# Kernel tuning notes

Measured on AMD Instinct MI355X. Metric: run time of the kernel, lower is better.

The kernel has to match this reference:

```python
import jax, jax.numpy as jnp
import numpy as np
from jax import lax

T, B, V, N = 128, 256, 256, 1024


def setup_inputs() -> dict:
    key = jax.random.key(0)
    k1, k2, k3, k4 = jax.random.split(key, 4)
    inputs = jax.random.uniform(k1, (T, B, V), dtype=jnp.float32)
    labels = jax.random.uniform(k2, (T * B, V), dtype=jnp.float32)
    weights = jax.random.normal(k3, (V + N, N), dtype=jnp.float32) * 0.1
    bias = jnp.zeros((N,), dtype=jnp.float32)
    output_weights = jax.random.normal(k4, (N, V), dtype=jnp.float32) * 0.1
    output_bias = jnp.zeros((V,), dtype=jnp.float32)
    return {
        "inputs": inputs,
        "labels": labels,
        "weights": weights,
        "bias": bias,
        "output_weights": output_weights,
        "output_bias": output_bias,
    }


def reference(inputs, labels, weights, bias, output_weights, output_bias):
    t, b, v = inputs.shape
    n = weights.shape[1]
    # split concat-matmul into x@Wx + h@Wh (same math as concat([x,h]) @ W)
    w_x = weights[:v]   # [V, N]
    w_h = weights[v:]   # [N, N]

    def step(h, x):
        h_new = jnp.tanh(x @ w_x + h @ w_h + bias)
        return h_new, h_new

    h0 = jnp.zeros((b, n), dtype=inputs.dtype)
    _, outputs = lax.scan(step, h0, inputs)          # [T, B, N]
    outputs = outputs.reshape(t * b, n)              # concat over time
    logits = outputs @ output_weights + output_bias  # [T*B, V]
    # softmax_cross_entropy_with_logits (soft labels), then mean
    log_p = jax.nn.log_softmax(logits, axis=-1)
    loss = jnp.mean(-jnp.sum(labels * log_p, axis=-1))
    return loss
```

## Files before the change

kernel.cpp:

```cpp
#include <hip/hip_runtime.h>
#include <math.h>

typedef __bf16 bf16;
typedef __attribute__((ext_vector_type(4))) __bf16 bf16x4;
typedef __attribute__((ext_vector_type(8))) __bf16 bf16x8;
typedef __attribute__((ext_vector_type(4))) float f32x4;

#define T_STEPS 128
#define B_SZ    256
#define V_SZ    256
#define N_SZ    1024
#define NROWS   (T_STEPS * B_SZ)
#define LDSS    72
#define RSTR    68
#define NGRP    16
#define NCB     16

__device__ __forceinline__ float fast_tanh(float x) {
    float e = __expf(2.0f * x);
    return 1.0f - 2.0f / (e + 1.0f);
}

__global__ void k_convert(const float* __restrict__ src, bf16* __restrict__ dst, int n) {
    int i = (blockIdx.x * blockDim.x + threadIdx.x) * 4;
    if (i < n) {
        float4 v = *(const float4*)(src + i);
        bf16x4 o;
        o.x = (bf16)v.x; o.y = (bf16)v.y; o.z = (bf16)v.z; o.w = (bf16)v.w;
        *(bf16x4*)(dst + i) = o;
    }
}

__global__ void k_transpose_cvt(const float* __restrict__ src, bf16* __restrict__ dst,
                                int R, int C) {
    __shared__ float tile[32][33];
    int c0 = blockIdx.x * 32;
    int r0 = blockIdx.y * 32;
    int tx = threadIdx.x & 31;
    int ty = threadIdx.x >> 5;
#pragma unroll
    for (int i = 0; i < 32; i += 8)
        tile[ty + i][tx] = src[(size_t)(r0 + ty + i) * C + c0 + tx];
    __syncthreads();
#pragma unroll
    for (int i = 0; i < 32; i += 8)
        dst[(size_t)(c0 + ty + i) * R + r0 + tx] = (bf16)tile[tx][ty + i];
}

__global__ __launch_bounds__(256) void k_xproj(
    const bf16* __restrict__ X, const bf16* __restrict__ Wxt,
    const float* __restrict__ bias, bf16* __restrict__ XH)
{
    __shared__ __align__(16) bf16 As[64 * LDSS];
    __shared__ __align__(16) bf16 Bs[64 * LDSS];
    const int tid  = threadIdx.x;
    const int lane = tid & 63;
    const int w    = tid >> 6;
    const int wm   = (w >> 1) * 32;
    const int wn   = (w & 1) * 32;
    const int quad = lane >> 4;
    const int l15  = lane & 15;
    const int m0 = blockIdx.x * 64;
    const int n0 = blockIdx.y * 64;

    const bf16* Ag = X + (size_t)m0 * V_SZ;
    const bf16* Bg = Wxt + (size_t)n0 * V_SZ;

    f32x4 z = {0.f, 0.f, 0.f, 0.f};
    f32x4 acc00 = z, acc01 = z, acc10 = z, acc11 = z;

    for (int k0 = 0; k0 < V_SZ; k0 += 64) {
        {
            int c = tid, row = c >> 3, col = (c & 7) * 8;
            *(bf16x8*)&As[row * LDSS + col] = *(const bf16x8*)&Ag[(size_t)row * V_SZ + k0 + col];
            *(bf16x8*)&Bs[row * LDSS + col] = *(const bf16x8*)&Bg[(size_t)row * V_SZ + k0 + col];
            c = tid + 256; row = c >> 3; col = (c & 7) * 8;
            *(bf16x8*)&As[row * LDSS + col] = *(const bf16x8*)&Ag[(size_t)row * V_SZ + k0 + col];
            *(bf16x8*)&Bs[row * LDSS + col] = *(const bf16x8*)&Bg[(size_t)row * V_SZ + k0 + col];
        }
        __syncthreads();
#pragma unroll
        for (int kc = 0; kc < 64; kc += 32) {
            bf16x8 a0 = *(const bf16x8*)&As[(wm + l15) * LDSS + kc + quad * 8];
            bf16x8 a1 = *(const bf16x8*)&As[(wm + 16 + l15) * LDSS + kc + quad * 8];
            bf16x8 b0 = *(const bf16x8*)&Bs[(wn + l15) * LDSS + kc + quad * 8];
            bf16x8 b1 = *(const bf16x8*)&Bs[(wn + 16 + l15) * LDSS + kc + quad * 8];
            acc00 = __builtin_amdgcn_mfma_f32_16x16x32_bf16(a0, b0, acc00, 0, 0, 0);
            acc01 = __builtin_amdgcn_mfma_f32_16x16x32_bf16(a0, b1, acc01, 0, 0, 0);
            acc10 = __builtin_amdgcn_mfma_f32_16x16x32_bf16(a1, b0, acc10, 0, 0, 0);
            acc11 = __builtin_amdgcn_mfma_f32_16x16x32_bf16(a1, b1, acc11, 0, 0, 0);
        }
        __syncthreads();
    }
    bf16* Out = XH + (size_t)m0 * N_SZ + n0;
    const f32x4 accs[2][2] = {{acc00, acc01}, {acc10, acc11}};
#pragma unroll
    for (int mi = 0; mi < 2; ++mi)
#pragma unroll
        for (int r = 0; r < 4; ++r) {
            int row = wm + mi * 16 + quad * 4 + r;
            bool is_t0 = (m0 + row) < B_SZ;
#pragma unroll
            for (int ni = 0; ni < 2; ++ni) {
                int col = wn + ni * 16 + l15;
                float pre = accs[mi][ni][r] + bias[n0 + col];
                if (is_t0) pre = fast_tanh(pre);
                Out[(size_t)row * N_SZ + col] = (bf16)pre;
            }
        }
}

__global__ __launch_bounds__(512, 2) void k_rnn(
    const bf16* __restrict__ Wht,
    bf16* __restrict__ XH,
    int* __restrict__ cnt)
{
    __shared__ float red[8 * 16 * RSTR];
    const int tid  = threadIdx.x;
    const int lane = tid & 63;
    const int w    = tid >> 6;
    const int quad = lane >> 4;
    const int l15  = lane & 15;
    const int g  = blockIdx.x >> 4;
    const int c  = blockIdx.x & 15;
    const int m0 = g * 16;
    const int n0 = c * 64;
    const int k0 = w * 128;

    const bf16* Bp = Wht + (size_t)(n0 + l15) * N_SZ + k0 + quad * 8;
    bf16x8 b[4][4];
#pragma unroll
    for (int nt = 0; nt < 4; ++nt)
#pragma unroll
        for (int kc = 0; kc < 4; ++kc)
            b[nt][kc] = *(const bf16x8*)&Bp[(size_t)(nt * 16) * N_SZ + kc * 32];

    const int orow = tid >> 5;
    const int ocol = (tid & 31) * 2;
    uint* XHu = (uint*)XH;

    for (int t = 1; t < T_STEPS; ++t) {
        size_t oidx = (((size_t)t * B_SZ + m0 + orow) * N_SZ + n0 + ocol) >> 1;
        uint xw = __hip_atomic_load(&XHu[oidx], __ATOMIC_RELAXED,
                                    __HIP_MEMORY_SCOPE_AGENT);

        if (t > 1) {
            if (tid == 0) {
                while (__hip_atomic_load(&cnt[g * T_STEPS + t - 1],
                                         __ATOMIC_RELAXED, __HIP_MEMORY_SCOPE_AGENT) < NCB)
                    __builtin_amdgcn_s_sleep(2);
            }
            __syncthreads();
        }

        const bf16* Ap = XH + ((size_t)(t - 1) * B_SZ + m0 + l15) * N_SZ + k0 + quad * 8;
        bf16x8 a[4];
#pragma unroll
        for (int kc = 0; kc < 4; ++kc)
            a[kc] = *(const bf16x8*)&Ap[kc * 32];

        f32x4 z = {0.f, 0.f, 0.f, 0.f};
        f32x4 acc[4] = {z, z, z, z};
#pragma unroll
        for (int kc = 0; kc < 4; ++kc)
#pragma unroll
            for (int nt = 0; nt < 4; ++nt)
                acc[nt] = __builtin_amdgcn_mfma_f32_16x16x32_bf16(a[kc], b[nt][kc],
                                                                  acc[nt], 0, 0, 0);

#pragma unroll
        for (int nt = 0; nt < 4; ++nt)
#pragma unroll
            for (int r = 0; r < 4; ++r)
                red[(w * 16 + quad * 4 + r) * RSTR + nt * 16 + l15] = acc[nt][r];
        __syncthreads();

        float s0 = 0.f, s1 = 0.f;
#pragma unroll
        for (int w2 = 0; w2 < 8; ++w2) {
            float2 v = *(const float2*)&red[(w2 * 16 + orow) * RSTR + ocol];
            s0 += v.x; s1 += v.y;
        }
        bf16 x0 = __builtin_bit_cast(bf16, (unsigned short)(xw & 0xffff));
        bf16 x1 = __builtin_bit_cast(bf16, (unsigned short)(xw >> 16));
        bf16 r0 = (bf16)fast_tanh(s0 + (float)x0);
        bf16 r1 = (bf16)fast_tanh(s1 + (float)x1);
        uint outw = (uint)__builtin_bit_cast(unsigned short, r0)
                  | ((uint)__builtin_bit_cast(unsigned short, r1) << 16);
        __hip_atomic_store(&XHu[oidx], outw, __ATOMIC_RELAXED,
                           __HIP_MEMORY_SCOPE_AGENT);

        asm volatile("s_waitcnt vmcnt(0)" ::: "memory");
        __syncthreads();
        if (tid == 0)
            __hip_atomic_fetch_add(&cnt[g * T_STEPS + t], 1,
                                   __ATOMIC_RELAXED, __HIP_MEMORY_SCOPE_AGENT);
    }
}

__global__ __launch_bounds__(512, 4) void k_loss(
    const bf16* __restrict__ XH,
    const bf16* __restrict__ Wot,
    const float* __restrict__ ob,
    const float* __restrict__ labels,
    float* __restrict__ out)
{
    __shared__ __align__(16) bf16 As[128 * LDSS];
    __shared__ __align__(16) bf16 Bs[256 * LDSS];
    const int tid  = threadIdx.x;
    const int lane = tid & 63;
    const int w    = tid >> 6;
    const int quad = lane >> 4;
    const int l15  = lane & 15;
    const int m0 = blockIdx.x * 128;

    f32x4 z = {0.f, 0.f, 0.f, 0.f};
    f32x4 acc[16];
#pragma unroll
    for (int i = 0; i < 16; ++i) acc[i] = z;

    const bf16* Ag = XH + (size_t)m0 * N_SZ;
    for (int k0 = 0; k0 < N_SZ; k0 += 64) {
#pragma unroll
        for (int c = tid; c < 1024; c += 512) {
            int row = c >> 3, col = (c & 7) * 8;
            *(bf16x8*)&As[row * LDSS + col] = *(const bf16x8*)&Ag[(size_t)row * N_SZ + k0 + col];
        }
#pragma unroll
        for (int c = tid; c < 2048; c += 512) {
            int row = c >> 3, col = (c & 7) * 8;
            *(bf16x8*)&Bs[row * LDSS + col] = *(const bf16x8*)&Wot[(size_t)row * N_SZ + k0 + col];
        }
        __syncthreads();
#pragma unroll
        for (int kc = 0; kc < 64; kc += 32) {
            bf16x8 a = *(const bf16x8*)&As[(w * 16 + l15) * LDSS + kc + quad * 8];
#pragma unroll
            for (int nt = 0; nt < 16; ++nt) {
                bf16x8 b = *(const bf16x8*)&Bs[(nt * 16 + l15) * LDSS + kc + quad * 8];
                acc[nt] = __builtin_amdgcn_mfma_f32_16x16x32_bf16(a, b, acc[nt], 0, 0, 0);
            }
        }
        __syncthreads();
    }

    float obv[16];
#pragma unroll
    for (int nt = 0; nt < 16; ++nt) obv[nt] = ob[nt * 16 + l15];

    float total = 0.f;
#pragma unroll
    for (int r = 0; r < 4; ++r) {
        int row = m0 + w * 16 + quad * 4 + r;
        float vals[16];
        float lmax = -3.0e38f;
#pragma unroll
        for (int nt = 0; nt < 16; ++nt) {
            vals[nt] = acc[nt][r] + obv[nt];
            lmax = fmaxf(lmax, vals[nt]);
        }
#pragma unroll
        for (int s = 1; s < 16; s <<= 1)
            lmax = fmaxf(lmax, __shfl_xor(lmax, s, 64));
        float sume = 0.f, labv = 0.f, labs = 0.f;
        const float* lrow = labels + (size_t)row * V_SZ;
#pragma unroll
        for (int nt = 0; nt < 16; ++nt) {
            sume += __expf(vals[nt] - lmax);
            float lb = lrow[nt * 16 + l15];
            labv += lb * vals[nt];
            labs += lb;
        }
#pragma unroll
        for (int s = 1; s < 16; s <<= 1) {
            sume += __shfl_xor(sume, s, 64);
            labv += __shfl_xor(labv, s, 64);
            labs += __shfl_xor(labs, s, 64);
        }
        float lse = lmax + __logf(sume);
        total += labs * lse - labv;
    }
    if (l15 == 0)
        atomicAdd(out, total * (1.0f / (float)NROWS));
}

extern "C" void kernel_launch(void* const* d_in, const int* in_sizes, int n_in,
                              void* d_out, int out_size, void* d_ws, size_t ws_size,
                              hipStream_t stream)
{
    const float* inputs  = (const float*)d_in[0];
    const float* labels  = (const float*)d_in[1];
    const float* weights = (const float*)d_in[2];
    const float* bias    = (const float*)d_in[3];
    const float* out_w   = (const float*)d_in[4];
    const float* out_b   = (const float*)d_in[5];
    float* out = (float*)d_out;

    char* ws = (char*)d_ws;
    bf16* XH  = (bf16*)ws;  ws += (size_t)NROWS * N_SZ * 2;
    bf16* Xb  = (bf16*)ws;  ws += (size_t)NROWS * V_SZ * 2;
    bf16* Wxt = (bf16*)ws;  ws += (size_t)N_SZ * V_SZ * 2;
    bf16* Wht = (bf16*)ws;  ws += (size_t)N_SZ * N_SZ * 2;
    bf16* Wot = (bf16*)ws;  ws += (size_t)V_SZ * N_SZ * 2;
    int*  cnt = (int*)ws;   ws += (size_t)NGRP * T_STEPS * 4;

    hipMemsetAsync(out, 0, sizeof(float), stream);
    hipMemsetAsync(cnt, 0, (size_t)NGRP * T_STEPS * 4, stream);

    k_convert<<<dim3(NROWS * V_SZ / 1024), 256, 0, stream>>>(inputs, Xb, NROWS * V_SZ);
    k_transpose_cvt<<<dim3(N_SZ / 32, V_SZ / 32), 256, 0, stream>>>(weights, Wxt, V_SZ, N_SZ);
    k_transpose_cvt<<<dim3(N_SZ / 32, N_SZ / 32), 256, 0, stream>>>(
        weights + (size_t)V_SZ * N_SZ, Wht, N_SZ, N_SZ);
    k_transpose_cvt<<<dim3(V_SZ / 32, N_SZ / 32), 256, 0, stream>>>(out_w, Wot, N_SZ, V_SZ);

    k_xproj<<<dim3(NROWS / 64, N_SZ / 64), 256, 0, stream>>>(Xb, Wxt, bias, XH);

    k_rnn<<<dim3(NGRP * NCB), 512, 0, stream>>>(Wht, XH, cnt);

    k_loss<<<dim3(NROWS / 128), 512, 0, stream>>>(XH, Wot, out_b, labels, out);
}
```

Before: 561.1 us.

## Fuse input projection and output logits GEMM into persistent RNN kernel

Removes the separate input-projection GEMM and the output-projection GEMM. Each recurrent block now computes x@Wx on the fly from register-held Wx slices, and uses idle time after publishing h_t to compute the logits slice of h_{t-1}@Wo. The logits go to a bf16 buffer that a lightweight softmax-cross-entropy kernel then reduces. The intent is to cut DRAM traffic and kernel launches by using the latency-bound recurrence's spare compute. The cost is more register pressure and extra LDS reductions and barriers inside every step of the serial loop, plus rounding the logits to bf16.

Result: faster. 502.2 us (-10.5%).

```diff
diff --git a/kernel.cpp b/kernel.cpp
--- a/kernel.cpp
+++ b/kernel.cpp
@@ -11,8 +11,8 @@
 #define V_SZ    256
 #define N_SZ    1024
 #define NROWS   (T_STEPS * B_SZ)
-#define LDSS    72
 #define RSTR    68
+#define LSTR    17
 #define NGRP    16
 #define NCB     16
 
@@ -47,75 +47,18 @@
         dst[(size_t)(c0 + ty + i) * R + r0 + tx] = (bf16)tile[tx][ty + i];
 }
 
-__global__ __launch_bounds__(256) void k_xproj(
-    const bf16* __restrict__ X, const bf16* __restrict__ Wxt,
-    const float* __restrict__ bias, bf16* __restrict__ XH)
-{
-    __shared__ __align__(16) bf16 As[64 * LDSS];
-    __shared__ __align__(16) bf16 Bs[64 * LDSS];
-    const int tid  = threadIdx.x;
-    const int lane = tid & 63;
-    const int w    = tid >> 6;
-    const int wm   = (w >> 1) * 32;
-    const int wn   = (w & 1) * 32;
-    const int quad = lane >> 4;
-    const int l15  = lane & 15;
-    const int m0 = blockIdx.x * 64;
-    const int n0 = blockIdx.y * 64;
-
-    const bf16* Ag = X + (size_t)m0 * V_SZ;
-    const bf16* Bg = Wxt + (size_t)n0 * V_SZ;
-
-    f32x4 z = {0.f, 0.f, 0.f, 0.f};
-    f32x4 acc00 = z, acc01 = z, acc10 = z, acc11 = z;
-
-    for (int k0 = 0; k0 < V_SZ; k0 += 64) {
-        {
-            int c = tid, row = c >> 3, col = (c & 7) * 8;
-            *(bf16x8*)&As[row * LDSS + col] = *(const bf16x8*)&Ag[(size_t)row * V_SZ + k0 + col];
-            *(bf16x8*)&Bs[row * LDSS + col] = *(const bf16x8*)&Bg[(size_t)row * V_SZ + k0 + col];
-            c = tid + 256; row = c >> 3; col = (c & 7) * 8;
-            *(bf16x8*)&As[row * LDSS + col] = *(const bf16x8*)&Ag[(size_t)row * V_SZ + k0 + col];
-            *(bf16x8*)&Bs[row * LDSS + col] = *(const bf16x8*)&Bg[(size_t)row * V_SZ + k0 + col];
-        }
-        __syncthreads();
-#pragma unroll
-        for (int kc = 0; kc < 64; kc += 32) {
-            bf16x8 a0 = *(const bf16x8*)&As[(wm + l15) * LDSS + kc + quad * 8];
-            bf16x8 a1 = *(const bf16x8*)&As[(wm + 16 + l15) * LDSS + kc + quad * 8];
-            bf16x8 b0 = *(const bf16x8*)&Bs[(wn + l15) * LDSS + kc + quad * 8];
-            bf16x8 b1 = *(const bf16x8*)&Bs[(wn + 16 + l15) * LDSS + kc + quad * 8];
-            acc00 = __builtin_amdgcn_mfma_f32_16x16x32_bf16(a0, b0, acc00, 0, 0, 0);
-            acc01 = __builtin_amdgcn_mfma_f32_16x16x32_bf16(a0, b1, acc01, 0, 0, 0);
-            acc10 = __builtin_amdgcn_mfma_f32_16x16x32_bf16(a1, b0, acc10, 0, 0, 0);
-            acc11 = __builtin_amdgcn_mfma_f32_16x16x32_bf16(a1, b1, acc11, 0, 0, 0);
-        }
-        __syncthreads();
-    }
-    bf16* Out = XH + (size_t)m0 * N_SZ + n0;
-    const f32x4 accs[2][2] = {{acc00, acc01}, {acc10, acc11}};
-#pragma unroll
-    for (int mi = 0; mi < 2; ++mi)
-#pragma unroll
-        for (int r = 0; r < 4; ++r) {
-            int row = wm + mi * 16 + quad * 4 + r;
-            bool is_t0 = (m0 + row) < B_SZ;
-#pragma unroll
-            for (int ni = 0; ni < 2; ++ni) {
-                int col = wn + ni * 16 + l15;
-                float pre = accs[mi][ni][r] + bias[n0 + col];
-                if (is_t0) pre = fast_tanh(pre);
-                Out[(size_t)row * N_SZ + col] = (bf16)pre;
-            }
-        }
-}
-
 __global__ __launch_bounds__(512, 2) void k_rnn(
+    const bf16* __restrict__ Xb,
+    const bf16* __restrict__ Wxt,
     const bf16* __restrict__ Wht,
+    const bf16* __restrict__ Wot,
+    const float* __restrict__ bias,
     bf16* __restrict__ XH,
+    unsigned int* __restrict__ Lgu,
     int* __restrict__ cnt)
 {
     __shared__ float red[8 * 16 * RSTR];
+    __shared__ float lred[8 * 16 * LSTR];
     const int tid  = threadIdx.x;
     const int lane = tid & 63;
     const int w    = tid >> 6;
@@ -126,6 +69,7 @@
     const int m0 = g * 16;
     const int n0 = c * 64;
     const int k0 = w * 128;
+    const int v0 = w * 32;
 
     const bf16* Bp = Wht + (size_t)(n0 + l15) * N_SZ + k0 + quad * 8;
     bf16x8 b[4][4];
@@ -134,24 +78,62 @@
 #pragma unroll
         for (int kc = 0; kc < 4; ++kc)
             b[nt][kc] = *(const bf16x8*)&Bp[(size_t)(nt * 16) * N_SZ + kc * 32];
+    bf16x8 bx[4];
+#pragma unroll
+    for (int nt = 0; nt < 4; ++nt)
+        bx[nt] = *(const bf16x8*)&Wxt[(size_t)(n0 + nt * 16 + l15) * V_SZ + v0 + quad * 8];
+    bf16x8 bo[4];
+#pragma unroll
+    for (int kc = 0; kc < 4; ++kc)
+        bo[kc] = *(const bf16x8*)&Wot[(size_t)(c * 16 + l15) * N_SZ + k0 + kc * 32 + quad * 8];
 
     const int orow = tid >> 5;
     const int ocol = (tid & 31) * 2;
-    uint* XHu = (uint*)XH;
+    const float bias0 = bias[n0 + ocol];
+    const float bias1 = bias[n0 + ocol + 1];
+    unsigned int* XHu = (unsigned int*)XH;
+    const f32x4 zz = {0.f, 0.f, 0.f, 0.f};
+
+    {
+        bf16x8 ax = *(const bf16x8*)&Xb[(size_t)(m0 + l15) * V_SZ + v0 + quad * 8];
+        f32x4 acc[4] = {zz, zz, zz, zz};
+#pragma unroll
+        for (int nt = 0; nt < 4; ++nt)
+            acc[nt] = __builtin_amdgcn_mfma_f32_16x16x32_bf16(ax, bx[nt], acc[nt], 0, 0, 0);
+#pragma unroll
+        for (int nt = 0; nt < 4; ++nt)
+#pragma unroll
+            for (int r = 0; r < 4; ++r)
+                red[(w * 16 + quad * 4 + r) * RSTR + nt * 16 + l15] = acc[nt][r];
+        __syncthreads();
+        float s0 = bias0, s1 = bias1;
+#pragma unroll
+        for (int w2 = 0; w2 < 8; ++w2) {
+            float2 v = *(const float2*)&red[(w2 * 16 + orow) * RSTR + ocol];
+            s0 += v.x; s1 += v.y;
+        }
+        bf16 r0 = (bf16)fast_tanh(s0);
+        bf16 r1 = (bf16)fast_tanh(s1);
+        unsigned int outw = (unsigned int)__builtin_bit_cast(unsigned short, r0)
+                          | ((unsigned int)__builtin_bit_cast(unsigned short, r1) << 16);
+        size_t oidx = (((size_t)0 * B_SZ + m0 + orow) * N_SZ + n0 + ocol) >> 1;
+        __hip_atomic_store(&XHu[oidx], outw, __ATOMIC_RELAXED, __HIP_MEMORY_SCOPE_AGENT);
+        asm volatile("s_waitcnt vmcnt(0)" ::: "memory");
+        __syncthreads();
+        if (tid == 0)
+            __hip_atomic_fetch_add(&cnt[g * T_STEPS + 0], 1,
+                                   __ATOMIC_RELAXED, __HIP_MEMORY_SCOPE_AGENT);
+    }
 
     for (int t = 1; t < T_STEPS; ++t) {
-        size_t oidx = (((size_t)t * B_SZ + m0 + orow) * N_SZ + n0 + ocol) >> 1;
-        uint xw = __hip_atomic_load(&XHu[oidx], __ATOMIC_RELAXED,
-                                    __HIP_MEMORY_SCOPE_AGENT);
-
-        if (t > 1) {
-            if (tid == 0) {
-                while (__hip_atomic_load(&cnt[g * T_STEPS + t - 1],
-                                         __ATOMIC_RELAXED, __HIP_MEMORY_SCOPE_AGENT) < NCB)
-                    __builtin_amdgcn_s_sleep(2);
-            }
-            __syncthreads();
-        }
+        bf16x8 ax = *(const bf16x8*)&Xb[((size_t)t * B_SZ + m0 + l15) * V_SZ + v0 + quad * 8];
+
+        if (tid == 0) {
+            while (__hip_atomic_load(&cnt[g * T_STEPS + t - 1],
+                                     __ATOMIC_RELAXED, __HIP_MEMORY_SCOPE_AGENT) < NCB)
+                __builtin_amdgcn_s_sleep(2);
+        }
+        __syncthreads();
 
         const bf16* Ap = XH + ((size_t)(t - 1) * B_SZ + m0 + l15) * N_SZ + k0 + quad * 8;
         bf16x8 a[4];
@@ -159,8 +141,10 @@
         for (int kc = 0; kc < 4; ++kc)
             a[kc] = *(const bf16x8*)&Ap[kc * 32];
 
-        f32x4 z = {0.f, 0.f, 0.f, 0.f};
-        f32x4 acc[4] = {z, z, z, z};
+        f32x4 acc[4] = {zz, zz, zz, zz};
+#pragma unroll
+        for (int nt = 0; nt < 4; ++nt)
+            acc[nt] = __builtin_amdgcn_mfma_f32_16x16x32_bf16(ax, bx[nt], acc[nt], 0, 0, 0);
 #pragma unroll
         for (int kc = 0; kc < 4; ++kc)
 #pragma unroll
@@ -175,113 +159,129 @@
                 red[(w * 16 + quad * 4 + r) * RSTR + nt * 16 + l15] = acc[nt][r];
         __syncthreads();
 
-        float s0 = 0.f, s1 = 0.f;
+        float s0 = bias0, s1 = bias1;
 #pragma unroll
         for (int w2 = 0; w2 < 8; ++w2) {
             float2 v = *(const float2*)&red[(w2 * 16 + orow) * RSTR + ocol];
             s0 += v.x; s1 += v.y;
         }
-        bf16 x0 = __builtin_bit_cast(bf16, (unsigned short)(xw & 0xffff));
-        bf16 x1 = __builtin_bit_cast(bf16, (unsigned short)(xw >> 16));
-        bf16 r0 = (bf16)fast_tanh(s0 + (float)x0);
-        bf16 r1 = (bf16)fast_tanh(s1 + (float)x1);
-        uint outw = (uint)__builtin_bit_cast(unsigned short, r0)
-                  | ((uint)__builtin_bit_cast(unsigned short, r1) << 16);
-        __hip_atomic_store(&XHu[oidx], outw, __ATOMIC_RELAXED,
-                           __HIP_MEMORY_SCOPE_AGENT);
-
+        bf16 r0 = (bf16)fast_tanh(s0);
+        bf16 r1 = (bf16)fast_tanh(s1);
+        unsigned int outw = (unsigned int)__builtin_bit_cast(unsigned short, r0)
+                          | ((unsigned int)__builtin_bit_cast(unsigned short, r1) << 16);
+        size_t oidx = (((size_t)t * B_SZ + m0 + orow) * N_SZ + n0 + ocol) >> 1;
+        __hip_atomic_store(&XHu[oidx], outw, __ATOMIC_RELAXED, __HIP_MEMORY_SCOPE_AGENT);
         asm volatile("s_waitcnt vmcnt(0)" ::: "memory");
         __syncthreads();
         if (tid == 0)
             __hip_atomic_fetch_add(&cnt[g * T_STEPS + t], 1,
                                    __ATOMIC_RELAXED, __HIP_MEMORY_SCOPE_AGENT);
-    }
-}
-
-__global__ __launch_bounds__(512, 4) void k_loss(
-    const bf16* __restrict__ XH,
-    const bf16* __restrict__ Wot,
+
+        f32x4 lacc = zz;
+#pragma unroll
+        for (int kc = 0; kc < 4; ++kc)
+            lacc = __builtin_amdgcn_mfma_f32_16x16x32_bf16(a[kc], bo[kc], lacc, 0, 0, 0);
+#pragma unroll
+        for (int r = 0; r < 4; ++r)
+            lred[(w * 16 + quad * 4 + r) * LSTR + l15] = lacc[r];
+        __syncthreads();
+        if (tid < 128) {
+            int row = tid >> 3, vp = tid & 7;
+            float sa = 0.f, sb = 0.f;
+#pragma unroll
+            for (int w2 = 0; w2 < 8; ++w2) {
+                sa += lred[(w2 * 16 + row) * LSTR + vp * 2];
+                sb += lred[(w2 * 16 + row) * LSTR + vp * 2 + 1];
+            }
+            bf16 pa = (bf16)sa, pb = (bf16)sb;
+            unsigned int pw = (unsigned int)__builtin_bit_cast(unsigned short, pa)
+                            | ((unsigned int)__builtin_bit_cast(unsigned short, pb) << 16);
+            Lgu[(((size_t)(t - 1) * 16 + c) * B_SZ + m0 + row) * 8 + vp] = pw;
+        }
+        __syncthreads();
+    }
+
+    if (tid == 0) {
+        while (__hip_atomic_load(&cnt[g * T_STEPS + T_STEPS - 1],
+                                 __ATOMIC_RELAXED, __HIP_MEMORY_SCOPE_AGENT) < NCB)
+            __builtin_amdgcn_s_sleep(2);
+    }
+    __syncthreads();
+    {
+        const bf16* Ap = XH + ((size_t)(T_STEPS - 1) * B_SZ + m0 + l15) * N_SZ + k0 + quad * 8;
+        bf16x8 a[4];
+#pragma unroll
+        for (int kc = 0; kc < 4; ++kc)
+            a[kc] = *(const bf16x8*)&Ap[kc * 32];
+        f32x4 lacc = zz;
+#pragma unroll
+        for (int kc = 0; kc < 4; ++kc)
+            lacc = __builtin_amdgcn_mfma_f32_16x16x32_bf16(a[kc], bo[kc], lacc, 0, 0, 0);
+#pragma unroll
+        for (int r = 0; r < 4; ++r)
+            lred[(w * 16 + quad * 4 + r) * LSTR + l15] = lacc[r];
+        __syncthreads();
+        if (tid < 128) {
+            int row = tid >> 3, vp = tid & 7;
+            float sa = 0.f, sb = 0.f;
+#pragma unroll
+            for (int w2 = 0; w2 < 8; ++w2) {
+                sa += lred[(w2 * 16 + row) * LSTR + vp * 2];
+                sb += lred[(w2 * 16 + row) * LSTR + vp * 2 + 1];
+            }
+            bf16 pa = (bf16)sa, pb = (bf16)sb;
+            unsigned int pw = (unsigned int)__builtin_bit_cast(unsigned short, pa)
+                            | ((unsigned int)__builtin_bit_cast(unsigned short, pb) << 16);
+            Lgu[(((size_t)(T_STEPS - 1) * 16 + c) * B_SZ + m0 + row) * 8 + vp] = pw;
+        }
+    }
+}
+
+__global__ __launch_bounds__(256) void k_lred(
+    const bf16* __restrict__ Lg,
+    const float* __restrict__ labels,
     const float* __restrict__ ob,
-    const float* __restrict__ labels,
     float* __restrict__ out)
 {
-    __shared__ __align__(16) bf16 As[128 * LDSS];
-    __shared__ __align__(16) bf16 Bs[256 * LDSS];
+    __shared__ float bt[4];
     const int tid  = threadIdx.x;
     const int lane = tid & 63;
     const int w    = tid >> 6;
-    const int quad = lane >> 4;
-    const int l15  = lane & 15;
-    const int m0 = blockIdx.x * 128;
-
-    f32x4 z = {0.f, 0.f, 0.f, 0.f};
-    f32x4 acc[16];
-#pragma unroll
-    for (int i = 0; i < 16; ++i) acc[i] = z;
-
-    const bf16* Ag = XH + (size_t)m0 * N_SZ;
-    for (int k0 = 0; k0 < N_SZ; k0 += 64) {
-#pragma unroll
-        for (int c = tid; c < 1024; c += 512) {
-            int row = c >> 3, col = (c & 7) * 8;
-            *(bf16x8*)&As[row * LDSS + col] = *(const bf16x8*)&Ag[(size_t)row * N_SZ + k0 + col];
-        }
-#pragma unroll
-        for (int c = tid; c < 2048; c += 512) {
-            int row = c >> 3, col = (c & 7) * 8;
-            *(bf16x8*)&Bs[row * LDSS + col] = *(const bf16x8*)&Wot[(size_t)row * N_SZ + k0 + col];
-        }
-        __syncthreads();
-#pragma unroll
-        for (int kc = 0; kc < 64; kc += 32) {
-            bf16x8 a = *(const bf16x8*)&As[(w * 16 + l15) * LDSS + kc + quad * 8];
-#pragma unroll
-            for (int nt = 0; nt < 16; ++nt) {
-                bf16x8 b = *(const bf16x8*)&Bs[(nt * 16 + l15) * LDSS + kc + quad * 8];
-                acc[nt] = __builtin_amdgcn_mfma_f32_16x16x32_bf16(a, b, acc[nt], 0, 0, 0);
-            }
-        }
-        __syncthreads();
-    }
-
-    float obv[16];
-#pragma unroll
-    for (int nt = 0; nt < 16; ++nt) obv[nt] = ob[nt * 16 + l15];
-
-    float total = 0.f;
-#pragma unroll
-    for (int r = 0; r < 4; ++r) {
-        int row = m0 + w * 16 + quad * 4 + r;
-        float vals[16];
-        float lmax = -3.0e38f;
-#pragma unroll
-        for (int nt = 0; nt < 16; ++nt) {
-            vals[nt] = acc[nt][r] + obv[nt];
-            lmax = fmaxf(lmax, vals[nt]);
-        }
-#pragma unroll
-        for (int s = 1; s < 16; s <<= 1)
-            lmax = fmaxf(lmax, __shfl_xor(lmax, s, 64));
-        float sume = 0.f, labv = 0.f, labs = 0.f;
-        const float* lrow = labels + (size_t)row * V_SZ;
-#pragma unroll
-        for (int nt = 0; nt < 16; ++nt) {
-            sume += __expf(vals[nt] - lmax);
-            float lb = lrow[nt * 16 + l15];
-            labv += lb * vals[nt];
-            labs += lb;
-        }
-#pragma unroll
-        for (int s = 1; s < 16; s <<= 1) {
+    const int cs   = lane >> 2;
+    const int vi   = (lane & 3) * 4;
+    const float4 ob4 = *(const float4*)&ob[cs * 16 + vi];
+
+    float wtot = 0.f;
+    for (int i = 0; i < 32; ++i) {
+        int row  = blockIdx.x * 128 + w * 32 + i;
+        int p    = row >> 8;
+        int brow = row & 255;
+        bf16x4 lv = *(const bf16x4*)&Lg[(((size_t)p * 16 + cs) * B_SZ + brow) * 16 + vi];
+        float l0 = (float)lv.x + ob4.x;
+        float l1 = (float)lv.y + ob4.y;
+        float l2 = (float)lv.z + ob4.z;
+        float l3 = (float)lv.w + ob4.w;
+        float mx = fmaxf(fmaxf(l0, l1), fmaxf(l2, l3));
+#pragma unroll
+        for (int s = 1; s < 64; s <<= 1)
+            mx = fmaxf(mx, __shfl_xor(mx, s, 64));
+        float sume = __expf(l0 - mx) + __expf(l1 - mx) + __expf(l2 - mx) + __expf(l3 - mx);
+        const float4 lb = *(const float4*)&labels[(size_t)row * V_SZ + cs * 16 + vi];
+        float labs = lb.x + lb.y + lb.z + lb.w;
+        float labv = lb.x * l0 + lb.y * l1 + lb.z * l2 + lb.w * l3;
+#pragma unroll
+        for (int s = 1; s < 64; s <<= 1) {
             sume += __shfl_xor(sume, s, 64);
+            labs += __shfl_xor(labs, s, 64);
             labv += __shfl_xor(labv, s, 64);
-            labs += __shfl_xor(labs, s, 64);
-        }
-        float lse = lmax + __logf(sume);
-        total += labs * lse - labv;
-    }
-    if (l15 == 0)
-        atomicAdd(out, total * (1.0f / (float)NROWS));
+        }
+        float lse = mx + __logf(sume);
+        wtot += labs * lse - labv;
+    }
+    if (lane == 0) bt[w] = wtot;
+    __syncthreads();
+    if (tid == 0)
+        atomicAdd(out, (bt[0] + bt[1] + bt[2] + bt[3]) * (1.0f / (float)NROWS));
 }
 
 extern "C" void kernel_launch(void* const* d_in, const int* in_sizes, int n_in,
@@ -299,6 +299,7 @@
     char* ws = (char*)d_ws;
     bf16* XH  = (bf16*)ws;  ws += (size_t)NROWS * N_SZ * 2;
     bf16* Xb  = (bf16*)ws;  ws += (size_t)NROWS * V_SZ * 2;
+    bf16* Lg  = (bf16*)ws;  ws += (size_t)NROWS * V_SZ * 2;
     bf16* Wxt = (bf16*)ws;  ws += (size_t)N_SZ * V_SZ * 2;
     bf16* Wht = (bf16*)ws;  ws += (size_t)N_SZ * N_SZ * 2;
     bf16* Wot = (bf16*)ws;  ws += (size_t)V_SZ * N_SZ * 2;
@@ -313,9 +314,8 @@
         weights + (size_t)V_SZ * N_SZ, Wht, N_SZ, N_SZ);
     k_transpose_cvt<<<dim3(V_SZ / 32, N_SZ / 32), 256, 0, stream>>>(out_w, Wot, N_SZ, V_SZ);
 
-    k_xproj<<<dim3(NROWS / 64, N_SZ / 64), 256, 0, stream>>>(Xb, Wxt, bias, XH);
-
-    k_rnn<<<dim3(NGRP * NCB), 512, 0, stream>>>(Wht, XH, cnt);
-
-    k_loss<<<dim3(NROWS / 128), 512, 0, stream>>>(XH, Wot, out_b, labels, out);
-}
+    k_rnn<<<dim3(NGRP * NCB), 512, 0, stream>>>(Xb, Wxt, Wht, Wot, bias, XH,
+                                                (unsigned int*)Lg, cnt);
+
+    k_lred<<<dim3(NROWS / 128), 256, 0, stream>>>(Lg, labels, out_b, out);
+}
```
